# Optimization experiments

Hardware: AMD Instinct MI355X
Metric: run time of the kernel (lower is better)

## Reference

```python
import jax, jax.numpy as jnp
import numpy as np

N_NODES = 100000
N_EDGES = 3200000
NUM_CLASSES = 10
SQRT3 = 3.0 ** 0.5


def setup_inputs() -> dict:
    key = jax.random.key(0)
    ks = jax.random.split(key, 20)
    f32 = jnp.float32
    return {
        "positions": jax.random.normal(ks[0], (N_NODES, 3), f32) * 5.0,
        "edge_src": jax.random.randint(ks[1], (N_EDGES,), 0, N_NODES, jnp.int32),
        "edge_dst": jax.random.randint(ks[2], (N_EDGES,), 0, N_NODES, jnp.int32),
        # layer1: TP('1x0e', sh) -> '1x0e + 1x1o' -> Linear -> '5x0e + 5x1o'
        "W0_1": jax.random.normal(ks[3], (5, 1), f32),
        "W1_1": jax.random.normal(ks[4], (5, 1, 3), f32),
        "b_1": jax.random.normal(ks[5], (5,), f32),
        # gate1: Linear('5x0e+5x1o' -> '10x0e') uses only the 5 input 0e irreps
        "Wg1": jax.random.normal(ks[6], (10, 5), f32),
        "bg1": jax.random.normal(ks[7], (10,), f32),
        # layer2: TP('5x0e+5x1o', sh) -> 10x0e + 10x1o (+5x1e unused) -> '5x0e+5x1o'
        "W0_2": jax.random.normal(ks[8], (5, 10), f32),
        "W1_2": jax.random.normal(ks[9], (5, 10, 3), f32),
        "b_2": jax.random.normal(ks[10], (5,), f32),
        "Wg2": jax.random.normal(ks[11], (10, 5), f32),
        "bg2": jax.random.normal(ks[12], (10,), f32),
        # layer3: TP -> 10x0e used -> '5x0e'
        "W0_3": jax.random.normal(ks[13], (5, 10), f32),
        "b_3": jax.random.normal(ks[14], (5,), f32),
        "Wg3": jax.random.normal(ks[15], (10, 5), f32),
        "bg3": jax.random.normal(ks[16], (10,), f32),
        "Wout": jax.random.normal(ks[17], (NUM_CLASSES, 5), f32) * 0.3,
        "bout": jax.random.normal(ks[18], (NUM_CLASSES,), f32) * 0.1,
    }


def _sh1(rel):
    # component-normalized real spherical harmonics, lmax=1: Y0 = 1, Y1 = sqrt(3)*r_hat
    r = jnp.linalg.norm(rel, axis=-1, keepdims=True)
    return SQRT3 * rel / jnp.maximum(r, 1e-9)  # [E,3]


def _scatter_mean(x, dst, n):
    s = jax.ops.segment_sum(x, dst, num_segments=n)
    cnt = jax.ops.segment_sum(jnp.ones((x.shape[0],), x.dtype), dst, num_segments=n)
    cnt = jnp.maximum(cnt, 1.0).reshape((n,) + (1,) * (x.ndim - 1))
    return s / cnt


def _layer(s, v, sh1, dst, n, W0, b, W1=None):
    # per-edge CG tensor product of dest-node features with edge SH, then linear, then scatter-mean
    sd = s[dst]                                            # [E,a0] gather 0e feats
    tp_s = [sd]                                            # 0e x 0e(Y0=1) -> 0e
    if v is not None:
        vd = v[dst]                                        # [E,a1,3] gather 1o feats
        tp_s.append(jnp.einsum('eic,ec->ei', vd, sh1) / SQRT3)  # 1o x 1o -> 0e (CG dot)
    tp_s = jnp.concatenate(tp_s, axis=1)
    out_s = _scatter_mean(tp_s @ W0.T + b, dst, n)         # [N,out0]
    if W1 is None:
        return out_s, None
    tp_v = [sd[:, :, None] * sh1[:, None, :]]              # 0e x 1o -> 1o
    if v is not None:
        tp_v.append(vd)                                    # 1o x 0e(Y0=1) -> 1o
    tp_v = jnp.concatenate(tp_v, axis=1)                   # [E,in1,3]
    out_v = _scatter_mean(jnp.einsum('eic,oic->eoc', tp_v, W1), dst, n)
    return out_s, out_v


def _gate(s, v, Wg, bg):
    # ActivationLayer: gate each irrep by GELU of a learned scalar (torch GELU = exact erf)
    g = jax.nn.gelu(s @ Wg.T + bg, approximate=False)
    n0 = s.shape[1]
    gs = g[:, :n0] * s
    if v is None:
        return gs, None
    return gs, g[:, n0:n0 + v.shape[1], None] * v


def reference(positions, edge_src, edge_dst, W0_1, W1_1, b_1, Wg1, bg1,
              W0_2, W1_2, b_2, Wg2, bg2, W0_3, b_3, Wg3, bg3, Wout, bout):
    n = positions.shape[0]
    rel = positions[edge_dst] - positions[edge_src]
    sh1 = _sh1(rel)
    s = jnp.ones((n, 1), positions.dtype)  # dummy '1x0e' starting node features
    s, v = _layer(s, None, sh1, edge_dst, n, W0_1, b_1, W1_1)
    s, v = _gate(s, v, Wg1, bg1)
    s, v = _layer(s, v, sh1, edge_dst, n, W0_2, b_2, W1_2)
    s, v = _gate(s, v, Wg2, bg2)
    s, _ = _layer(s, v, sh1, edge_dst, n, W0_3, b_3, None)
    s, _ = _gate(s, None, Wg3, bg3)
    pooled = jnp.mean(s, axis=0)                       # avg over nodes -> [5]
    return jax.nn.softmax(pooled @ Wout.T + bout)      # [NUM_CLASSES]
```

## Files before the change

### kernel.cpp

```cpp
#include <hip/hip_runtime.h>
#include <math.h>

#define SQRT3F 1.7320508075688772f
#define INV_SQRT3F 0.57735026918962576f
typedef unsigned long long u64;
typedef unsigned int u32;

#define PK_SCALE 1024.0f
#define PK_MASK  0x7FFFFull

#define NPR2   2048
#define NRG2   49
#define REP2   ((size_t)NRG2 * NPR2)
#define EPB    4096
#define OVF_CAP 131072

#define NPR    4096
#define NRANGE 25

__device__ __forceinline__ float gelu_exact(float x) {
    return 0.5f * x * (1.0f + erff(x * 0.70710678118654752f));
}

__device__ __forceinline__ u64 sh_to_w(float rx, float ry, float rz) {
    float rr = sqrtf(rx*rx + ry*ry + rz*rz);
    float inv = (SQRT3F * PK_SCALE) / fmaxf(rr, 1e-9f);
    u32 ax = (u32)__float2int_rn(rx * inv) + 2048u;
    u32 ay = (u32)__float2int_rn(ry * inv) + 2048u;
    u32 az = (u32)__float2int_rn(rz * inv) + 2048u;
    return (u64)ax | ((u64)ay << 19) | ((u64)az << 38) | (1ull << 57);
}

__global__ __launch_bounds__(256) void pack_pos_kernel(
    const float* __restrict__ pos, float4* __restrict__ pos4,
    u64* __restrict__ ovf_cnt, u32* __restrict__ done, int N)
{
    int i = blockIdx.x * 256 + threadIdx.x;
    if (i < N) pos4[i] = make_float4(pos[3*i], pos[3*i+1], pos[3*i+2], 0.f);
    if (blockIdx.x == 0 && threadIdx.x == 0) { *ovf_cnt = 0; *done = 0; }
}

__global__ __launch_bounds__(1024) void scatter_kernel(
    const int* __restrict__ src, const int* __restrict__ dst,
    u32* __restrict__ buckets, u32* __restrict__ cnts,
    u32* __restrict__ ovf_rec, u32* __restrict__ ovf_node, u64* __restrict__ ovf_cnt,
    int E, int CAP)
{
    __shared__ u32 scnt[NRG2];
    const int p = blockIdx.x;
    if (threadIdx.x < NRG2) scnt[threadIdx.x] = 0;
    __syncthreads();

    const int start = p * EPB;
    int end = start + EPB;
    if (end > E) end = E;
    u32* const bkt = buckets + (size_t)p * NRG2 * (size_t)CAP;

    int i0 = start + (int)threadIdx.x * 4;
    if (i0 + 4 <= end) {
        int4 d4 = *reinterpret_cast<const int4*>(dst + i0);
        int4 s4 = *reinterpret_cast<const int4*>(src + i0);
        int d[4] = {d4.x, d4.y, d4.z, d4.w};
        int s[4] = {s4.x, s4.y, s4.z, s4.w};
        u32 rec[4]; int r[4];
        #pragma unroll
        for (int k = 0; k < 4; ++k) {
            r[k] = d[k] >> 11;
            rec[k] = ((u32)s[k] << 11) | ((u32)d[k] & 2047u);
        }
        u32 slot[4];
        #pragma unroll
        for (int k = 0; k < 4; ++k) slot[k] = atomicAdd(&scnt[r[k]], 1u);
        #pragma unroll
        for (int k = 0; k < 4; ++k) {
            if (slot[k] < (u32)CAP) {
                bkt[(size_t)r[k] * CAP + slot[k]] = rec[k];
            } else {
                u64 os = atomicAdd(ovf_cnt, 1ull);
                if (os < OVF_CAP) { ovf_rec[os] = rec[k]; ovf_node[os] = (u32)d[k]; }
            }
        }
    } else if (i0 < end) {
        for (int i = i0; i < end; ++i) {
            int dd = dst[i], ss = src[i];
            int r = dd >> 11;
            u32 rec = ((u32)ss << 11) | ((u32)dd & 2047u);
            u32 slot = atomicAdd(&scnt[r], 1u);
            if (slot < (u32)CAP) bkt[(size_t)r * CAP + slot] = rec;
            else {
                u64 os = atomicAdd(ovf_cnt, 1ull);
                if (os < OVF_CAP) { ovf_rec[os] = rec; ovf_node[os] = (u32)dd; }
            }
        }
    }
    __syncthreads();
    if (threadIdx.x < NRG2) {
        u32 c = scnt[threadIdx.x];
        cnts[p * NRG2 + threadIdx.x] = c < (u32)CAP ? c : (u32)CAP;
    }
}

__global__ __launch_bounds__(512) void gather_kernel(
    const float4* __restrict__ pos4,
    const u32* __restrict__ buckets, const u32* __restrict__ cnts,
    const u32* __restrict__ ovf_rec, const u32* __restrict__ ovf_node,
    const u64* __restrict__ ovf_cnt,
    u64* __restrict__ reps, int P, int CAP, int R2, int N)
{
    __shared__ u64 bins[NPR2];
    __shared__ float4 posl[NPR2];
    __shared__ u32 segn[128];
    const int r  = blockIdx.x % NRG2;
    const int c2 = blockIdx.x / NRG2;
    const int base = r * NPR2;

    for (int j = threadIdx.x; j < NPR2; j += 512) {
        bins[j] = 0;
        int g = base + j;
        posl[j] = (g < N) ? pos4[g] : make_float4(0.f, 0.f, 0.f, 0.f);
    }
    const int nseg = (P - c2 + R2 - 1) / R2;
    for (int t = threadIdx.x; t < nseg; t += 512)
        segn[t] = cnts[(c2 + t * R2) * NRG2 + r];
    __syncthreads();

    const int wid = threadIdx.x >> 6, lane = threadIdx.x & 63;
    for (int sgi = wid; sgi < nseg; sgi += 8) {
        const int p = c2 + sgi * R2;
        const u32 n = segn[sgi];
        const u32* seg = buckets + ((size_t)p * NRG2 + r) * (size_t)CAP;
        for (u32 t = lane; t < n; t += 64) {
            u32 rec = seg[t];
            u32 j = rec & 2047u, s = rec >> 11;
            float4 ps = pos4[s];
            float4 pd = posl[j];
            atomicAdd(&bins[j], sh_to_w(pd.x - ps.x, pd.y - ps.y, pd.z - ps.z));
        }
    }
    if (c2 == 0) {
        u64 n = *ovf_cnt; if (n > OVF_CAP) n = OVF_CAP;
        for (u64 t = threadIdx.x; t < n; t += 512) {
            u32 dd = ovf_node[t];
            if ((int)(dd >> 11) == r) {
                u32 rec = ovf_rec[t];
                u32 j = rec & 2047u, s = rec >> 11;
                float4 ps = pos4[s]; float4 pd = posl[j];
                atomicAdd(&bins[j], sh_to_w(pd.x - ps.x, pd.y - ps.y, pd.z - ps.z));
            }
        }
    }
    __syncthreads();

    u64* outp = reps + (size_t)c2 * REP2 + base;
    for (int j = threadIdx.x; j < NPR2; j += 512) outp[j] = bins[j];
}

__global__ __launch_bounds__(256, 4) void edge_bin_kernel(
    const float* __restrict__ pos,
    const int* __restrict__ src,
    const int* __restrict__ dst,
    u64* __restrict__ reps, int E, int span)
{
    __shared__ u64 bins[NPR];
    __shared__ u32 q[4][128];
    const int g = blockIdx.x;
    const int xcd = g & 7;
    const int slot = g >> 3;
    const int c = xcd + 8 * (slot / NRANGE);
    const int r = slot % NRANGE;
    const int base = r * NPR;
    const int lane = threadIdx.x & 63;
    const int wid  = threadIdx.x >> 6;
    const u64 ltmask = (1ull << lane) - 1ull;

    for (int j = threadIdx.x; j < NPR; j += 256) bins[j] = 0;
    __syncthreads();

    const int start = c * span;
    int end = start + span;
    if (end > E) end = E;
    const int niter = (end > start) ? ((end - start + 1023) >> 10) : 0;
    int qcount = 0;

    auto process = [&](u32 i2) {
        int s2 = src[i2]; int d2 = dst[i2];
        u32 j = (u32)(d2 - base);
        atomicAdd(&bins[j], sh_to_w(pos[3*d2+0]-pos[3*s2+0],
                                    pos[3*d2+1]-pos[3*s2+1],
                                    pos[3*d2+2]-pos[3*s2+2]));
    };

    for (int t = 0; t < niter; ++t) {
        int i0 = start + ((int)threadIdx.x << 2) + (t << 10);
        int4 d4 = make_int4(-1, -1, -1, -1);
        if (i0 + 4 <= end) d4 = *reinterpret_cast<const int4*>(dst + i0);
        else if (i0 < end) for (int k = 0; i0 + k < end; ++k) (&d4.x)[k] = dst[i0 + k];
        #pragma unroll
        for (int k = 0; k < 4; ++k) {
            int i = i0 + k;
            bool in = (i < end) && ((u32)((&d4.x)[k] - base) < NPR);
            u64 mask = __ballot(in);
            if (in) q[wid][qcount + __popcll(mask & ltmask)] = (u32)i;
            qcount += (int)__popcll(mask);
            if (qcount >= 64) { qcount -= 64; process(q[wid][qcount + lane]); }
        }
    }
    if (lane < qcount) process(q[wid][lane]);
    __syncthreads();

    u64* outp = reps + (size_t)c * ((size_t)NRANGE * NPR) + base;
    for (int j = threadIdx.x; j < NPR; j += 256) outp[j] = bins[j];
}

template<bool FUSE>
__global__ __launch_bounds__(256) void node_kernel(
    const u64* __restrict__ reps, size_t repStride, int R,
    const float* __restrict__ W0_1, const float* __restrict__ W1_1, const float* __restrict__ b_1,
    const float* __restrict__ Wg1,  const float* __restrict__ bg1,
    const float* __restrict__ W0_2, const float* __restrict__ W1_2, const float* __restrict__ b_2,
    const float* __restrict__ Wg2,  const float* __restrict__ bg2,
    const float* __restrict__ W0_3, const float* __restrict__ b_3,
    const float* __restrict__ Wg3,  const float* __restrict__ bg3,
    float* __restrict__ partials, int N,
    const float* __restrict__ Wout, const float* __restrict__ bout,
    float* __restrict__ out, float invN, u32* __restrict__ done)
{
    int d = blockIdx.x * blockDim.x + threadIdx.x;
    float sf[5] = {0.f, 0.f, 0.f, 0.f, 0.f};

    if (d < N) {
        u64 w = 0;
        int r = 0;
        for (; r + 4 <= R; r += 4) {
            u64 a0 = reps[(size_t)(r+0) * repStride + (u32)d];
            u64 a1 = reps[(size_t)(r+1) * repStride + (u32)d];
            u64 a2 = reps[(size_t)(r+2) * repStride + (u32)d];
            u64 a3 = reps[(size_t)(r+3) * repStride + (u32)d];
            w += a0 + a1 + a2 + a3;
        }
        for (; r < R; ++r) w += reps[(size_t)r * repStride + (u32)d];
        u32 deg = (u32)(w >> 57);
        if (deg > 0) {
            long long bias = (long long)deg << 11;
            float invdS = 1.0f / (PK_SCALE * (float)deg);
            float m[3];
            m[0] = (float)((long long)( w        & PK_MASK) - bias) * invdS;
            m[1] = (float)((long long)((w >> 19) & PK_MASK) - bias) * invdS;
            m[2] = (float)((long long)((w >> 38) & PK_MASK) - bias) * invdS;

            float s1[5], v1[5][3];
            #pragma unroll
            for (int i = 0; i < 5; ++i) {
                s1[i] = W0_1[i] + b_1[i];
                #pragma unroll
                for (int c = 0; c < 3; ++c) v1[i][c] = W1_1[i*3+c] * m[c];
            }
            float g1[10];
            #pragma unroll
            for (int j = 0; j < 10; ++j) {
                float t = bg1[j];
                #pragma unroll
                for (int i = 0; i < 5; ++i) t += Wg1[j*5+i] * s1[i];
                g1[j] = gelu_exact(t);
            }
            #pragma unroll
            for (int i = 0; i < 5; ++i) {
                s1[i] *= g1[i];
                #pragma unroll
                for (int c = 0; c < 3; ++c) v1[i][c] *= g1[5+i];
            }

            float dot1[5];
            #pragma unroll
            for (int i = 0; i < 5; ++i)
                dot1[i] = (v1[i][0]*m[0] + v1[i][1]*m[1] + v1[i][2]*m[2]) * INV_SQRT3F;
            float s2[5];
            #pragma unroll
            for (int o = 0; o < 5; ++o) {
                float t = b_2[o];
                #pragma unroll
                for (int i = 0; i < 5; ++i) t += W0_2[o*10+i] * s1[i];
                #pragma unroll
                for (int i = 0; i < 5; ++i) t += W0_2[o*10+5+i] * dot1[i];
                s2[o] = t;
            }
            float v2[5][3];
            #pragma unroll
            for (int o = 0; o < 5; ++o) {
                #pragma unroll
                for (int c = 0; c < 3; ++c) {
                    float t = 0.f;
                    #pragma unroll
                    for (int i = 0; i < 5; ++i) {
                        t += W1_2[(o*10+i)*3+c]   * (s1[i] * m[c]);
                        t += W1_2[(o*10+5+i)*3+c] * v1[i][c];
                    }
                    v2[o][c] = t;
                }
            }
            float g2[10];
            #pragma unroll
            for (int j = 0; j < 10; ++j) {
                float t = bg2[j];
                #pragma unroll
                for (int i = 0; i < 5; ++i) t += Wg2[j*5+i] * s2[i];
                g2[j] = gelu_exact(t);
            }
            #pragma unroll
            for (int i = 0; i < 5; ++i) {
                s2[i] *= g2[i];
                #pragma unroll
                for (int c = 0; c < 3; ++c) v2[i][c] *= g2[5+i];
            }

            float dot2[5];
            #pragma unroll
            for (int i = 0; i < 5; ++i)
                dot2[i] = (v2[i][0]*m[0] + v2[i][1]*m[1] + v2[i][2]*m[2]) * INV_SQRT3F;
            float s3[5];
            #pragma unroll
            for (int o = 0; o < 5; ++o) {
                float t = b_3[o];
                #pragma unroll
                for (int i = 0; i < 5; ++i) t += W0_3[o*10+i] * s2[i];
                #pragma unroll
                for (int i = 0; i < 5; ++i) t += W0_3[o*10+5+i] * dot2[i];
                s3[o] = t;
            }
            #pragma unroll
            for (int i = 0; i < 5; ++i) {
                float t = bg3[i];
                #pragma unroll
                for (int j = 0; j < 5; ++j) t += Wg3[i*5+j] * s3[j];
                sf[i] = gelu_exact(t) * s3[i];
            }
        }
    }

    #pragma unroll
    for (int k = 0; k < 5; ++k) {
        float v = sf[k];
        for (int off = 32; off > 0; off >>= 1) v += __shfl_down(v, off);
        sf[k] = v;
    }
    __shared__ float lred[4][5];
    __shared__ int islast;
    int wid = threadIdx.x >> 6, lane = threadIdx.x & 63;
    if (lane == 0) {
        #pragma unroll
        for (int k = 0; k < 5; ++k) lred[wid][k] = sf[k];
    }
    __syncthreads();
    if (threadIdx.x == 0) {
        #pragma unroll
        for (int k = 0; k < 5; ++k)
            partials[blockIdx.x * 5 + k] = lred[0][k] + lred[1][k] + lred[2][k] + lred[3][k];
    }

    if (FUSE) {
        if (threadIdx.x == 0) {
            __threadfence();
            u32 old = atomicAdd(done, 1u);
            islast = (old == gridDim.x - 1);
        }
        __syncthreads();
        if (!islast) return;
        __threadfence();
        float s[5] = {0.f, 0.f, 0.f, 0.f, 0.f};
        for (int b = threadIdx.x; b < (int)gridDim.x; b += 256) {
            #pragma unroll
            for (int k = 0; k < 5; ++k) s[k] += partials[b * 5 + k];
        }
        #pragma unroll
        for (int k = 0; k < 5; ++k) {
            float v = s[k];
            for (int off = 32; off > 0; off >>= 1) v += __shfl_down(v, off);
            s[k] = v;
        }
        __syncthreads();
        if (lane == 0) {
            #pragma unroll
            for (int k = 0; k < 5; ++k) lred[wid][k] = s[k];
        }
        __syncthreads();
        if (threadIdx.x == 0) {
            float pooled[5];
            #pragma unroll
            for (int i = 0; i < 5; ++i)
                pooled[i] = (lred[0][i] + lred[1][i] + lred[2][i] + lred[3][i]) * invN;
            float lg[10], mx = -1e30f;
            #pragma unroll
            for (int j = 0; j < 10; ++j) {
                float t = bout[j];
                #pragma unroll
                for (int i = 0; i < 5; ++i) t += Wout[j*5+i] * pooled[i];
                lg[j] = t;
                mx = fmaxf(mx, t);
            }
            float se = 0.f;
            #pragma unroll
            for (int j = 0; j < 10; ++j) { lg[j] = expf(lg[j] - mx); se += lg[j]; }
            float inv = 1.0f / se;
            #pragma unroll
            for (int j = 0; j < 10; ++j) out[j] = lg[j] * inv;
        }
    }
}

__global__ __launch_bounds__(256) void finalize_kernel(
    const float* __restrict__ partials, int nb,
    const float* __restrict__ Wout, const float* __restrict__ bout,
    float* __restrict__ out, float invN)
{
    float s[5] = {0.f, 0.f, 0.f, 0.f, 0.f};
    for (int b = threadIdx.x; b < nb; b += 256) {
        #pragma unroll
        for (int k = 0; k < 5; ++k) s[k] += partials[b * 5 + k];
    }
    #pragma unroll
    for (int k = 0; k < 5; ++k) {
        float v = s[k];
        for (int off = 32; off > 0; off >>= 1) v += __shfl_down(v, off);
        s[k] = v;
    }
    __shared__ float lred[4][5];
    int wid = threadIdx.x >> 6, lane = threadIdx.x & 63;
    if (lane == 0) {
        #pragma unroll
        for (int k = 0; k < 5; ++k) lred[wid][k] = s[k];
    }
    __syncthreads();
    if (threadIdx.x == 0) {
        float pooled[5];
        #pragma unroll
        for (int i = 0; i < 5; ++i)
            pooled[i] = (lred[0][i] + lred[1][i] + lred[2][i] + lred[3][i]) * invN;
        float lg[10], mx = -1e30f;
        #pragma unroll
        for (int j = 0; j < 10; ++j) {
            float t = bout[j];
            #pragma unroll
            for (int i = 0; i < 5; ++i) t += Wout[j*5+i] * pooled[i];
            lg[j] = t;
            mx = fmaxf(mx, t);
        }
        float se = 0.f;
        #pragma unroll
        for (int j = 0; j < 10; ++j) { lg[j] = expf(lg[j] - mx); se += lg[j]; }
        float inv = 1.0f / se;
        #pragma unroll
        for (int j = 0; j < 10; ++j) out[j] = lg[j] * inv;
    }
}

extern "C" void kernel_launch(void* const* d_in, const int* in_sizes, int n_in,
                              void* d_out, int out_size, void* d_ws, size_t ws_size,
                              hipStream_t stream) {
    const float* pos  = (const float*)d_in[0];
    const int*   esrc = (const int*)d_in[1];
    const int*   edst = (const int*)d_in[2];
    const float* W0_1 = (const float*)d_in[3];
    const float* W1_1 = (const float*)d_in[4];
    const float* b_1  = (const float*)d_in[5];
    const float* Wg1  = (const float*)d_in[6];
    const float* bg1  = (const float*)d_in[7];
    const float* W0_2 = (const float*)d_in[8];
    const float* W1_2 = (const float*)d_in[9];
    const float* b_2  = (const float*)d_in[10];
    const float* Wg2  = (const float*)d_in[11];
    const float* bg2  = (const float*)d_in[12];
    const float* W0_3 = (const float*)d_in[13];
    const float* b_3  = (const float*)d_in[14];
    const float* Wg3  = (const float*)d_in[15];
    const float* bg3  = (const float*)d_in[16];
    const float* Wout = (const float*)d_in[17];
    const float* bout = (const float*)d_in[18];

    const int N = in_sizes[0] / 3;
    const int E = in_sizes[1];
    const int nblocks = (N + 255) / 256;
    const int P = (E + EPB - 1) / EPB;

    {
        const int r2c[3] = {16, 8, 4};
        int mean = (EPB + NRG2 - 1) / NRG2;
        int slack = mean / 2 > 64 ? mean / 2 : 64;
        int CAP = ((mean + slack + 15) / 16) * 16;

        for (int a = 0; a < 3; ++a) {
            int R2 = r2c[a];
            size_t off = 16384;
            size_t o_ctr  = off; off += 256;
            size_t o_pos4 = off; off += ((size_t)N * 16 + 255) & ~(size_t)255;
            size_t o_reps = off; off += (size_t)R2 * REP2 * 8;
            size_t o_cnts = off; off += ((size_t)P * NRG2 * 4 + 255) & ~(size_t)255;
            size_t o_ovfn = off; off += (size_t)OVF_CAP * 4;
            size_t o_ovfr = off; off += (size_t)OVF_CAP * 4;
            size_t o_bkts = off; off += (size_t)P * NRG2 * CAP * 4;
            if (off > ws_size) continue;

            float*  partials = (float*)d_ws;
            u64*    ovf_cnt  = (u64*)((char*)d_ws + o_ctr);
            u32*    done     = (u32*)((char*)d_ws + o_ctr + 8);
            float4* pos4     = (float4*)((char*)d_ws + o_pos4);
            u64*    reps     = (u64*)((char*)d_ws + o_reps);
            u32*    cnts     = (u32*)((char*)d_ws + o_cnts);
            u32*    ovf_node = (u32*)((char*)d_ws + o_ovfn);
            u32*    ovf_rec  = (u32*)((char*)d_ws + o_ovfr);
            u32*    buckets  = (u32*)((char*)d_ws + o_bkts);

            pack_pos_kernel<<<nblocks, 256, 0, stream>>>(pos, pos4, ovf_cnt, done, N);
            scatter_kernel<<<P, 1024, 0, stream>>>(esrc, edst,
                buckets, cnts, ovf_rec, ovf_node, ovf_cnt, E, CAP);
            gather_kernel<<<NRG2 * R2, 512, 0, stream>>>(pos4, buckets, cnts,
                ovf_rec, ovf_node, ovf_cnt, reps, P, CAP, R2, N);
            node_kernel<true><<<nblocks, 256, 0, stream>>>(reps, REP2, R2,
                W0_1, W1_1, b_1, Wg1, bg1,
                W0_2, W1_2, b_2, Wg2, bg2,
                W0_3, b_3, Wg3, bg3,
                partials, N, Wout, bout, (float*)d_out, 1.0f / (float)N, done);
            return;
        }
    }

    {
        float* partials = (float*)d_ws;
        u64* reps = (u64*)((char*)d_ws + 16384);
        const size_t repStride = (size_t)NRANGE * NPR;
        size_t avail = ws_size > 16384 ? ws_size - 16384 : 0;
        int C = (int)(avail / (repStride * 8));
        if (C > 48) C = 48;
        C &= ~7;
        if (C >= 8) {
            int span = (int)((((size_t)E + C - 1) / C + 3) & ~(size_t)3);
            edge_bin_kernel<<<NRANGE * C, 256, 0, stream>>>(pos, esrc, edst, reps, E, span);
            node_kernel<false><<<nblocks, 256, 0, stream>>>(reps, repStride, C,
                W0_1, W1_1, b_1, Wg1, bg1,
                W0_2, W1_2, b_2, Wg2, bg2,
                W0_3, b_3, Wg3, bg3,
                partials, N, nullptr, nullptr, nullptr, 0.f, nullptr);
            finalize_kernel<<<1, 256, 0, stream>>>(partials, nblocks, Wout, bout,
                                                   (float*)d_out, 1.0f / (float)N);
        }
    }
}
```

Baseline: 78.15 us.

## Replace fixed-capacity edge buckets with per-block counting sort in shared memory

The scatter kernel now builds a histogram of destination ranges per 4096-edge block, takes a prefix sum, and places records into a shared-memory buffer sorted by range. It then writes that buffer out contiguously, along with packed base/count pairs per range. This removes the fixed-capacity bucket layout and the global overflow path, including its atomic counter and the extra pass gather runs on block 0. Writes become coalesced and the workspace gets smaller, at the cost of extra barriers, a serial 49-entry scan and 16KB of shared memory per block in the scatter kernel.

```diff
diff --git a/kernel.cpp b/kernel.cpp
--- a/kernel.cpp
+++ b/kernel.cpp
@@ -13,7 +13,6 @@
 #define NRG2   49
 #define REP2   ((size_t)NRG2 * NPR2)
 #define EPB    4096
-#define OVF_CAP 131072
 
 #define NPR    4096
 #define NRANGE 25
@@ -33,83 +32,79 @@
 
 __global__ __launch_bounds__(256) void pack_pos_kernel(
     const float* __restrict__ pos, float4* __restrict__ pos4,
-    u64* __restrict__ ovf_cnt, u32* __restrict__ done, int N)
+    u32* __restrict__ done, int N)
 {
     int i = blockIdx.x * 256 + threadIdx.x;
     if (i < N) pos4[i] = make_float4(pos[3*i], pos[3*i+1], pos[3*i+2], 0.f);
-    if (blockIdx.x == 0 && threadIdx.x == 0) { *ovf_cnt = 0; *done = 0; }
+    if (blockIdx.x == 0 && threadIdx.x == 0) *done = 0;
 }
 
 __global__ __launch_bounds__(1024) void scatter_kernel(
     const int* __restrict__ src, const int* __restrict__ dst,
-    u32* __restrict__ buckets, u32* __restrict__ cnts,
-    u32* __restrict__ ovf_rec, u32* __restrict__ ovf_node, u64* __restrict__ ovf_cnt,
-    int E, int CAP)
+    u32* __restrict__ gbuf, u32* __restrict__ cnts, int E)
 {
-    __shared__ u32 scnt[NRG2];
+    __shared__ u32 hist[NRG2];
+    __shared__ u32 base[NRG2];
+    __shared__ u32 place[NRG2];
+    __shared__ u32 recbuf[EPB];
     const int p = blockIdx.x;
-    if (threadIdx.x < NRG2) scnt[threadIdx.x] = 0;
+    if (threadIdx.x < NRG2) hist[threadIdx.x] = 0;
     __syncthreads();
 
     const int start = p * EPB;
     int end = start + EPB;
     if (end > E) end = E;
-    u32* const bkt = buckets + (size_t)p * NRG2 * (size_t)CAP;
-
+
+    int nk = 0;
+    int d[4], s[4], r[4];
+    u32 rec[4];
     int i0 = start + (int)threadIdx.x * 4;
     if (i0 + 4 <= end) {
         int4 d4 = *reinterpret_cast<const int4*>(dst + i0);
         int4 s4 = *reinterpret_cast<const int4*>(src + i0);
-        int d[4] = {d4.x, d4.y, d4.z, d4.w};
-        int s[4] = {s4.x, s4.y, s4.z, s4.w};
-        u32 rec[4]; int r[4];
-        #pragma unroll
-        for (int k = 0; k < 4; ++k) {
-            r[k] = d[k] >> 11;
-            rec[k] = ((u32)s[k] << 11) | ((u32)d[k] & 2047u);
-        }
-        u32 slot[4];
-        #pragma unroll
-        for (int k = 0; k < 4; ++k) slot[k] = atomicAdd(&scnt[r[k]], 1u);
-        #pragma unroll
-        for (int k = 0; k < 4; ++k) {
-            if (slot[k] < (u32)CAP) {
-                bkt[(size_t)r[k] * CAP + slot[k]] = rec[k];
-            } else {
-                u64 os = atomicAdd(ovf_cnt, 1ull);
-                if (os < OVF_CAP) { ovf_rec[os] = rec[k]; ovf_node[os] = (u32)d[k]; }
-            }
-        }
+        d[0]=d4.x; d[1]=d4.y; d[2]=d4.z; d[3]=d4.w;
+        s[0]=s4.x; s[1]=s4.y; s[2]=s4.z; s[3]=s4.w;
+        nk = 4;
     } else if (i0 < end) {
-        for (int i = i0; i < end; ++i) {
-            int dd = dst[i], ss = src[i];
-            int r = dd >> 11;
-            u32 rec = ((u32)ss << 11) | ((u32)dd & 2047u);
-            u32 slot = atomicAdd(&scnt[r], 1u);
-            if (slot < (u32)CAP) bkt[(size_t)r * CAP + slot] = rec;
-            else {
-                u64 os = atomicAdd(ovf_cnt, 1ull);
-                if (os < OVF_CAP) { ovf_rec[os] = rec; ovf_node[os] = (u32)dd; }
-            }
-        }
-    }
-    __syncthreads();
-    if (threadIdx.x < NRG2) {
-        u32 c = scnt[threadIdx.x];
-        cnts[p * NRG2 + threadIdx.x] = c < (u32)CAP ? c : (u32)CAP;
-    }
+        nk = end - i0;
+        for (int k = 0; k < nk; ++k) { d[k] = dst[i0+k]; s[k] = src[i0+k]; }
+    }
+    for (int k = 0; k < nk; ++k) {
+        r[k] = d[k] >> 11;
+        rec[k] = ((u32)s[k] << 11) | ((u32)d[k] & 2047u);
+    }
+    for (int k = 0; k < nk; ++k) atomicAdd(&hist[r[k]], 1u);
+    __syncthreads();
+
+    if (threadIdx.x == 0) {
+        u32 acc = 0;
+        for (int j = 0; j < NRG2; ++j) { base[j] = acc; acc += hist[j]; }
+    }
+    __syncthreads();
+    if (threadIdx.x < NRG2) place[threadIdx.x] = base[threadIdx.x];
+    __syncthreads();
+
+    for (int k = 0; k < nk; ++k) {
+        u32 idx = atomicAdd(&place[r[k]], 1u);
+        recbuf[idx] = rec[k];
+    }
+    __syncthreads();
+
+    const int total = end - start;
+    u32* out = gbuf + (size_t)p * EPB;
+    for (int j = threadIdx.x; j < total; j += 1024) out[j] = recbuf[j];
+    if (threadIdx.x < NRG2)
+        cnts[p * NRG2 + threadIdx.x] = (base[threadIdx.x] << 16) | hist[threadIdx.x];
 }
 
 __global__ __launch_bounds__(512) void gather_kernel(
     const float4* __restrict__ pos4,
-    const u32* __restrict__ buckets, const u32* __restrict__ cnts,
-    const u32* __restrict__ ovf_rec, const u32* __restrict__ ovf_node,
-    const u64* __restrict__ ovf_cnt,
-    u64* __restrict__ reps, int P, int CAP, int R2, int N)
+    const u32* __restrict__ gbuf, const u32* __restrict__ cnts,
+    u64* __restrict__ reps, int P, int R2, int N)
 {
     __shared__ u64 bins[NPR2];
     __shared__ float4 posl[NPR2];
-    __shared__ u32 segn[128];
+    __shared__ u32 segn[256];
     const int r  = blockIdx.x % NRG2;
     const int c2 = blockIdx.x / NRG2;
     const int base = r * NPR2;
@@ -127,26 +122,15 @@
     const int wid = threadIdx.x >> 6, lane = threadIdx.x & 63;
     for (int sgi = wid; sgi < nseg; sgi += 8) {
         const int p = c2 + sgi * R2;
-        const u32 n = segn[sgi];
-        const u32* seg = buckets + ((size_t)p * NRG2 + r) * (size_t)CAP;
+        const u32 bc = segn[sgi];
+        const u32 n = bc & 0xFFFFu;
+        const u32* seg = gbuf + (size_t)p * EPB + (bc >> 16);
         for (u32 t = lane; t < n; t += 64) {
             u32 rec = seg[t];
-            u32 j = rec & 2047u, s = rec >> 11;
-            float4 ps = pos4[s];
+            u32 j = rec & 2047u, ss = rec >> 11;
+            float4 ps = pos4[ss];
             float4 pd = posl[j];
             atomicAdd(&bins[j], sh_to_w(pd.x - ps.x, pd.y - ps.y, pd.z - ps.z));
-        }
-    }
-    if (c2 == 0) {
-        u64 n = *ovf_cnt; if (n > OVF_CAP) n = OVF_CAP;
-        for (u64 t = threadIdx.x; t < n; t += 512) {
-            u32 dd = ovf_node[t];
-            if ((int)(dd >> 11) == r) {
-                u32 rec = ovf_rec[t];
-                u32 j = rec & 2047u, s = rec >> 11;
-                float4 ps = pos4[s]; float4 pd = posl[j];
-                atomicAdd(&bins[j], sh_to_w(pd.x - ps.x, pd.y - ps.y, pd.z - ps.z));
-            }
         }
     }
     __syncthreads();
@@ -483,10 +467,6 @@
 
     {
         const int r2c[3] = {16, 8, 4};
-        int mean = (EPB + NRG2 - 1) / NRG2;
-        int slack = mean / 2 > 64 ? mean / 2 : 64;
-        int CAP = ((mean + slack + 15) / 16) * 16;
-
         for (int a = 0; a < 3; ++a) {
             int R2 = r2c[a];
             size_t off = 16384;
@@ -494,26 +474,20 @@
             size_t o_pos4 = off; off += ((size_t)N * 16 + 255) & ~(size_t)255;
             size_t o_reps = off; off += (size_t)R2 * REP2 * 8;
             size_t o_cnts = off; off += ((size_t)P * NRG2 * 4 + 255) & ~(size_t)255;
-            size_t o_ovfn = off; off += (size_t)OVF_CAP * 4;
-            size_t o_ovfr = off; off += (size_t)OVF_CAP * 4;
-            size_t o_bkts = off; off += (size_t)P * NRG2 * CAP * 4;
+            size_t o_gbuf = off; off += (size_t)P * EPB * 4;
             if (off > ws_size) continue;
 
             float*  partials = (float*)d_ws;
-            u64*    ovf_cnt  = (u64*)((char*)d_ws + o_ctr);
-            u32*    done     = (u32*)((char*)d_ws + o_ctr + 8);
+            u32*    done     = (u32*)((char*)d_ws + o_ctr);
             float4* pos4     = (float4*)((char*)d_ws + o_pos4);
             u64*    reps     = (u64*)((char*)d_ws + o_reps);
             u32*    cnts     = (u32*)((char*)d_ws + o_cnts);
-            u32*    ovf_node = (u32*)((char*)d_ws + o_ovfn);
-            u32*    ovf_rec  = (u32*)((char*)d_ws + o_ovfr);
-            u32*    buckets  = (u32*)((char*)d_ws + o_bkts);
-
-            pack_pos_kernel<<<nblocks, 256, 0, stream>>>(pos, pos4, ovf_cnt, done, N);
-            scatter_kernel<<<P, 1024, 0, stream>>>(esrc, edst,
-                buckets, cnts, ovf_rec, ovf_node, ovf_cnt, E, CAP);
-            gather_kernel<<<NRG2 * R2, 512, 0, stream>>>(pos4, buckets, cnts,
-                ovf_rec, ovf_node, ovf_cnt, reps, P, CAP, R2, N);
+            u32*    gbuf     = (u32*)((char*)d_ws + o_gbuf);
+
+            pack_pos_kernel<<<nblocks, 256, 0, stream>>>(pos, pos4, done, N);
+            scatter_kernel<<<P, 1024, 0, stream>>>(esrc, edst, gbuf, cnts, E);
+            gather_kernel<<<NRG2 * R2, 512, 0, stream>>>(pos4, gbuf, cnts,
+                reps, P, R2, N);
             node_kernel<true><<<nblocks, 256, 0, stream>>>(reps, REP2, R2,
                 W0_1, W1_1, b_1, Wg1, bg1,
                 W0_2, W1_2, b_2, Wg2, bg2,
```

Result: faster. 74.35 us (-4.9%).
